# Kernel optimization log

Hardware: AMD Instinct MI355X
Metric: run time of the kernel (lower is better)

The kernel has to match this reference:

```python
import jax, jax.numpy as jnp
import numpy as np
from jax import lax

ALPHA = 0.95
THRESH = 1.0
DN = ('NCDHW', 'OIDHW', 'NCDHW')  # (batch, chan, T, H, W)


def lif(x):
    # x: [B, C, T, H, W]. y[t] = (1-a)*y_reset[t-1] + x[t]; s = (y>=th); y *= (1-s)
    xt = jnp.moveaxis(x, 2, 0)  # [T, B, C, H, W]

    def step(y, x_t):
        y = (1.0 - ALPHA) * y + x_t
        s = (y >= THRESH).astype(x.dtype)
        return y * (1.0 - s), s

    _, s = lax.scan(step, jnp.zeros_like(xt[0]), xt)
    return jnp.moveaxis(s, 0, 2)  # back to [B, C, T, H, W]


def delta_encode(x):
    # temporal difference along T (axis 2), zero-padded at t=0
    d = x[:, :, 1:] - x[:, :, :-1]
    return jnp.concatenate([jnp.zeros_like(x[:, :, :1]), d], axis=2)


def setup_inputs() -> dict:
    key = jax.random.key(0)
    ks = jax.random.split(key, 7)
    B, H, W, T = 2, 64, 64, 350
    return {
        'x': jax.random.uniform(ks[0], (B, 2, H, W, T), dtype=jnp.float32),
        'conv1_w': jax.random.normal(ks[1], (8, 2, 5, 5, 1), dtype=jnp.float32) * 0.1,
        'conv1_b': jax.random.normal(ks[2], (8,), dtype=jnp.float32) * 0.1,
        'deconv_w': jax.random.normal(ks[3], (2, 8, 2, 2, 1), dtype=jnp.float32) * 0.1,
        'deconv_b': jax.random.normal(ks[4], (2,), dtype=jnp.float32) * 0.1,
        'conv2_w': jax.random.normal(ks[5], (2, 2), dtype=jnp.float32) * 0.1,
        'conv2_b': jax.random.normal(ks[6], (2,), dtype=jnp.float32) * 0.1,
    }


def reference(x, conv1_w, conv1_b, deconv_w, deconv_b, conv2_w, conv2_b):
    # x: [B, 2, H, W, T] -> [B, 2, T, H, W]
    h = jnp.transpose(x, (0, 1, 4, 2, 3))
    # conv1: kernel (5,5,1) over (T,H,W), padding (2,2,0)
    h = lax.conv_general_dilated(h, conv1_w, (1, 1, 1),
                                 [(2, 2), (2, 2), (0, 0)],
                                 dimension_numbers=DN)
    h = jax.nn.relu(h + conv1_b[None, :, None, None, None])
    h = lif(h)
    h = delta_encode(h)
    # deconv: kernel (2,2,1), stride (2,2,1) -> upsamples T and H by 2
    h = lax.conv_transpose(h, deconv_w, (2, 2, 1), 'VALID',
                           dimension_numbers=DN)
    h = h + deconv_b[None, :, None, None, None]
    # dropout3d(0.1) is identity in eval mode
    h = jax.nn.relu(h)
    # conv2: 1x1x1 conv == channel-mixing matmul
    h = jnp.einsum('oc,bcthw->bothw', conv2_w, h) + conv2_b[None, :, None, None, None]
    h = lif(h)
    # [B, C, T', H', W'] -> [B, C, H', W', T']
    return jnp.transpose(h, (0, 1, 3, 4, 2))
```

## Files before the change

### kernel.cpp

```cpp
#include <hip/hip_runtime.h>

constexpr int B  = 2,  CIN = 2,  H = 64, W = 64, T = 350;
constexpr int C1 = 8;
constexpr int TO = 700, HO = 128, WO = 64;
constexpr int HW = H * W;

#define DEC 0.05000000074505806f

__global__ void __launch_bounds__(256) transpose_kernel(
    const float* __restrict__ x, float* __restrict__ xT) {
  __shared__ float tile[64][65];
  int bid   = blockIdx.x;
  int tTile = bid % 6;
  int slice = bid / 6;
  int h  = slice % H;
  int bc = slice / H;
  int t0 = tTile * 64;
  int tx = threadIdx.x & 63;
  int tz = threadIdx.x >> 6;

  const float* src = x + ((long)bc * H + h) * (long)(W * T);
#pragma unroll
  for (int i = 0; i < 16; ++i) {
    int w = tz * 16 + i;
    int t = t0 + tx;
    tile[w][tx] = (t < T) ? src[(long)w * T + t] : 0.0f;
  }
  __syncthreads();
  float* dst = xT + ((long)bc * T) * HW + h * 64;
#pragma unroll
  for (int i = 0; i < 16; ++i) {
    int tl = tz * 16 + i;
    int t  = t0 + tl;
    if (t < T) dst[(long)t * HW + tx] = tile[tx][tl];
  }
}

__device__ __forceinline__ void gload_lds16(const float* g, float* l) {
  __builtin_amdgcn_global_load_lds(
      (const __attribute__((address_space(1))) unsigned int*)g,
      (__attribute__((address_space(3))) unsigned int*)l, 16, 0, 0);
}

__global__ void __launch_bounds__(512) convlif_kernel(
    const float* __restrict__ xT, const float* __restrict__ w1,
    const float* __restrict__ b1, signed char* __restrict__ d8) {
  __shared__ float buf[2][128 * 64];
  const int tid = threadIdx.x;
  const int bid = blockIdx.x;
  const int chunk = bid & 3;
  const int rest  = bid >> 2;
  const int h = rest & 63;
  const int b = rest >> 6;
  const int w  = tid & 63;
  const int co = tid >> 6;

  float wt[2][5][5];
#pragma unroll
  for (int ci = 0; ci < 2; ++ci)
#pragma unroll
    for (int dt = 0; dt < 5; ++dt)
#pragma unroll
      for (int dh = 0; dh < 5; ++dh)
        wt[ci][dt][dh] = w1[((co * 2 + ci) * 5 + dt) * 5 + dh];
  float bias = b1[co];

  const float* basep[2][5];
#pragma unroll
  for (int ci = 0; ci < 2; ++ci)
#pragma unroll
    for (int dh = 0; dh < 5; ++dh) {
      int hh = h + dh - 2;
      bool hv = (hh >= 0) && (hh < H);
      int hc = hh < 0 ? 0 : (hh > H - 1 ? H - 1 : hh);
      basep[ci][dh] = xT + ((long)((b * 2 + ci) * T)) * HW + hc * 64 + w;
      if (!hv) {
#pragma unroll
        for (int dt = 0; dt < 5; ++dt) wt[ci][dt][dh] = 0.0f;
      }
    }

  int tloc[4];
  int cpart[4];
#pragma unroll
  for (int i = 0; i < 4; ++i) {
    int r = (tid >> 4) + 32 * i;
    if (r > 99) r = 99;
    int tl  = r / 10;
    int rem = r - tl * 10;
    int ci  = rem / 5;
    int dh  = rem - ci * 5;
    int hh = h + dh - 2;
    int hc = hh < 0 ? 0 : (hh > H - 1 ? H - 1 : hh);
    tloc[i]  = tl;
    cpart[i] = ((b * 2 + ci) * T) * HW + hc * 64 + (tid & 15) * 4;
  }

  const int tstore = chunk * 88;
  const int ts     = chunk ? tstore - 15 : 0;
  const int te     = tstore + 88 < T ? tstore + 88 : T;
  const int nsup   = (te - ts + 9) / 10;

  {
    int bs = ts + 3;
#pragma unroll
    for (int i = 0; i < 4; ++i) {
      int tau = bs + tloc[i];
      if (tau > T - 1) tau = T - 1;
      gload_lds16(xT + (long)cpart[i] + (long)tau * HW,
                  &buf[0][(i * 32 + co * 4) * 64]);
    }
  }

  float win[2][5][5];
#pragma unroll
  for (int ci = 0; ci < 2; ++ci)
#pragma unroll
    for (int dh = 0; dh < 5; ++dh) {
      const float* bp = basep[ci][dh];
      win[ci][dh][3] = (ts >= 2) ? bp[(long)(ts - 2) * HW] : 0.0f;
      win[ci][dh][4] = (ts >= 1) ? bp[(long)(ts - 1) * HW] : 0.0f;
      win[ci][dh][0] = bp[(long)(ts + 0) * HW];
      win[ci][dh][1] = bp[(long)(ts + 1) * HW];
      win[ci][dh][2] = bp[(long)(ts + 2) * HW];
    }

  asm volatile("s_waitcnt vmcnt(0)" ::: "memory");
  __builtin_amdgcn_s_barrier();
  asm volatile("" ::: "memory");

  signed char* dsto = d8 + ((long)(b * T) * HW + h * 64 + w) * C1 + co;

  float y = 0.0f, sprev = 0.0f;
  for (int k = 0; k < nsup; ++k) {
    asm volatile("" ::: "memory");
    __builtin_amdgcn_s_barrier();
    asm volatile("" ::: "memory");
    if (k + 1 < nsup) {
      int bs = ts + 3 + 10 * (k + 1);
      float* nb = &buf[(k + 1) & 1][0];
#pragma unroll
      for (int i = 0; i < 4; ++i) {
        int tau = bs + tloc[i];
        if (tau > T - 1) tau = T - 1;
        gload_lds16(xT + (long)cpart[i] + (long)tau * HW,
                    nb + (i * 32 + co * 4) * 64);
      }
      asm volatile("s_waitcnt vmcnt(4)" ::: "memory");
    } else {
      asm volatile("s_waitcnt vmcnt(0)" ::: "memory");
    }
    __builtin_amdgcn_s_barrier();
    asm volatile("" ::: "memory");

    float* lb = &buf[k & 1][0];
    {
      int bufstart = ts + 3 + 10 * k;
      int rz0 = (T - bufstart) * 10;
      if (rz0 < 100) {
        if (rz0 < 0) rz0 = 0;
        for (int r = rz0 + co; r < 100; r += 8) lb[r * 64 + w] = 0.0f;
        asm volatile("" ::: "memory");
        __builtin_amdgcn_s_barrier();
        asm volatile("" ::: "memory");
      }
    }

    const int t0s = ts + 10 * k;
    for (int jj = 0; jj < 2; ++jj) {
#pragma unroll
      for (int u = 0; u < 5; ++u) {
        const int j5 = jj * 5;
        int t = t0s + j5 + u;
        float ac0 = 0.f, ac1 = 0.f, ac2 = 0.f, ac3 = 0.f;
#pragma unroll
        for (int ci = 0; ci < 2; ++ci)
#pragma unroll
          for (int dt = 0; dt < 5; ++dt) {
            const int slot = (u + dt + 3) % 5;
#pragma unroll
            for (int dh = 0; dh < 5; ++dh) {
              const int q = (ci * 25 + dt * 5 + dh) & 3;
              float p = win[ci][dh][slot] * wt[ci][dt][dh];
              if (q == 0) ac0 += p;
              else if (q == 1) ac1 += p;
              else if (q == 2) ac2 += p;
              else ac3 += p;
            }
          }
        float a = ((ac0 + ac1) + (ac2 + ac3)) + bias;
        a = fmaxf(a, 0.0f);
        y = fmaf(DEC, y, a);
        float s = (y >= 1.0f) ? 1.0f : 0.0f;
        if (t >= tstore && t < te) {
          float dlt = (t == 0) ? 0.0f : (s - sprev);
          dsto[(long)t * (HW * C1)] = (signed char)dlt;
        }
        sprev = s;
        y = (s != 0.0f) ? 0.0f : y;
        const int slot2 = (u + 3) % 5;
#pragma unroll
        for (int ci = 0; ci < 2; ++ci)
#pragma unroll
          for (int dh = 0; dh < 5; ++dh)
            win[ci][dh][slot2] = lb[((j5 + u) * 10 + ci * 5 + dh) * 64 + w];
      }
    }
  }
}

__global__ void __launch_bounds__(64) stage2_kernel(
    const signed char* __restrict__ d8, const float* __restrict__ dw,
    const float* __restrict__ db, const float* __restrict__ cw,
    const float* __restrict__ cb, float* __restrict__ out) {
  __shared__ float SB[2][64][17];
  int bid   = blockIdx.x;
  int chunk = bid & 15;
  int rest  = bid >> 4;
  int hp = rest & 127;
  int b  = rest >> 7;
  int wp = threadIdx.x;

  int h  = hp >> 1;
  int kh = 1 - (hp & 1);

  float dwk0[2][8], dwk1[2][8];
#pragma unroll
  for (int c = 0; c < 2; ++c)
#pragma unroll
    for (int ci = 0; ci < 8; ++ci) {
      dwk0[c][ci] = dw[((c * 8 + ci) * 2 + 0) * 2 + kh];
      dwk1[c][ci] = dw[((c * 8 + ci) * 2 + 1) * 2 + kh];
    }
  float db0 = db[0], db1 = db[1];
  float cw00 = cw[0], cw01 = cw[1], cw10 = cw[2], cw11 = cw[3];
  float cb0 = cb[0], cb1 = cb[1];

  int t0 = chunk * 44;
  int t1 = (t0 + 44 < TO) ? t0 + 44 : TO;
  int tw = (t0 - 16 > 0) ? t0 - 16 : 0;

  const signed char* dbase = d8 + (((long)b * T) * HW + h * 64 + wp) * C1;
  const long tstride = (long)HW * C1;
  float* outb = out + ((long)b * 2 * HO) * (long)(WO * TO);

  float y0 = 0.0f, y1 = 0.0f;
  uint2 dc = *reinterpret_cast<const uint2*>(dbase + (long)(tw >> 1) * tstride);
  for (int tp = tw; tp < t1; tp += 2) {
    int tn = (tp + 2 < t1) ? ((tp + 2) >> 1) : ((t1 - 1) >> 1);
    uint2 dn = *reinterpret_cast<const uint2*>(dbase + (long)tn * tstride);

    float dv[8];
#pragma unroll
    for (int ci = 0; ci < 4; ++ci) {
      dv[ci]     = (float)(signed char)((dc.x >> (8 * ci)) & 0xff);
      dv[ci + 4] = (float)(signed char)((dc.y >> (8 * ci)) & 0xff);
    }

#pragma unroll
    for (int par = 0; par < 2; ++par) {
      int tpp = tp + par;
      float v0 = db0, v1 = db1;
      if (par == 0) {
#pragma unroll
        for (int ci = 0; ci < 8; ++ci) {
          v0 = fmaf(dv[ci], dwk1[0][ci], v0);
          v1 = fmaf(dv[ci], dwk1[1][ci], v1);
        }
      } else {
#pragma unroll
        for (int ci = 0; ci < 8; ++ci) {
          v0 = fmaf(dv[ci], dwk0[0][ci], v0);
          v1 = fmaf(dv[ci], dwk0[1][ci], v1);
        }
      }
      v0 = fmaxf(v0, 0.0f);
      v1 = fmaxf(v1, 0.0f);
      float u0 = fmaf(cw00, v0, fmaf(cw01, v1, cb0));
      float u1 = fmaf(cw10, v0, fmaf(cw11, v1, cb1));
      y0 = fmaf(DEC, y0, u0);
      y1 = fmaf(DEC, y1, u1);
      float s0 = (y0 >= 1.0f) ? 1.0f : 0.0f;
      float s1 = (y1 >= 1.0f) ? 1.0f : 0.0f;
      y0 = (s0 != 0.0f) ? 0.0f : y0;
      y1 = (s1 != 0.0f) ? 0.0f : y1;

      if (tpp >= t0) {
        int k = (tpp - t0) & 15;
        SB[0][wp][k] = s0;
        SB[1][wp][k] = s1;
        if (par == 1 && (k == 15 || tpp == t1 - 1)) {
          __syncthreads();
          int Kc  = k + 1;
          int t0f = tpp - k;
#pragma unroll
          for (int o = 0; o < 2; ++o) {
            float* ob = outb + ((long)(o * HO + hp)) * (long)(WO * TO);
#pragma unroll
            for (int i = 0; i < 4; ++i) {
              int idx = (i << 6) + wp;
              int r   = idx >> 2;
              int c   = (idx & 3) << 2;
              if (c < Kc) {
                float4 vv;
                vv.x = SB[o][r][c + 0];
                vv.y = SB[o][r][c + 1];
                vv.z = SB[o][r][c + 2];
                vv.w = SB[o][r][c + 3];
                *reinterpret_cast<float4*>(ob + (long)r * TO + (t0f + c)) = vv;
              }
            }
          }
          __syncthreads();
        }
      }
    }
    dc = dn;
  }
}

extern "C" void kernel_launch(void* const* d_in, const int* in_sizes, int n_in,
                              void* d_out, int out_size, void* d_ws, size_t ws_size,
                              hipStream_t stream) {
  const float* x  = (const float*)d_in[0];
  const float* w1 = (const float*)d_in[1];
  const float* b1 = (const float*)d_in[2];
  const float* dw = (const float*)d_in[3];
  const float* db = (const float*)d_in[4];
  const float* cw = (const float*)d_in[5];
  const float* cb = (const float*)d_in[6];
  float* out = (float*)d_out;

  float* xT = (float*)d_ws;
  signed char* d8 = (signed char*)d_ws + (size_t)B * CIN * T * HW * 4;

  transpose_kernel<<<dim3(B * CIN * H * 6), dim3(256), 0, stream>>>(x, xT);
  convlif_kernel<<<dim3(B * H * 4), dim3(512), 0, stream>>>(xT, w1, b1, d8);
  stage2_kernel<<<dim3(B * HO * 16), dim3(64), 0, stream>>>(d8, dw, db, cw, cb, out);
}
```

Measured before the change: 121.6 us.

## Process two H rows and two output channels per thread in conv-LIF kernel

Each conv-LIF block now covers two adjacent H rows, and each thread computes two output channels, so every input tap loaded into registers feeds twice the FMAs. The LDS staging holds 6 H rows per channel instead of 5, letting both rows share one time window. Spike deltas are packed into an LDS staging tile and written to global memory as 16-byte vector stores, replacing scattered byte stores. The grid drops to 256 blocks, which lowers parallelism, and register pressure rises from the doubled weights and accumulators.

Result: faster. 104.0 us (-14.5%).

```diff
diff --git a/kernel.cpp b/kernel.cpp
--- a/kernel.cpp
+++ b/kernel.cpp
@@ -46,70 +46,60 @@
     const float* __restrict__ xT, const float* __restrict__ w1,
     const float* __restrict__ b1, signed char* __restrict__ d8) {
   __shared__ float buf[2][128 * 64];
+  __shared__ __align__(16) unsigned char st[10][1024];
   const int tid = threadIdx.x;
   const int bid = blockIdx.x;
   const int chunk = bid & 3;
   const int rest  = bid >> 2;
-  const int h = rest & 63;
-  const int b = rest >> 6;
+  const int h2 = rest & 31;
+  const int b  = rest >> 5;
+  const int h0 = h2 * 2;
   const int w  = tid & 63;
-  const int co = tid >> 6;
-
-  float wt[2][5][5];
-#pragma unroll
-  for (int ci = 0; ci < 2; ++ci)
-#pragma unroll
-    for (int dt = 0; dt < 5; ++dt)
-#pragma unroll
-      for (int dh = 0; dh < 5; ++dh)
-        wt[ci][dt][dh] = w1[((co * 2 + ci) * 5 + dt) * 5 + dh];
-  float bias = b1[co];
-
-  const float* basep[2][5];
+  const int hs = (tid >> 6) & 1;
+  const int cp = tid >> 7;
+  const int h  = h0 + hs;
+  const int wid = tid >> 6;
+
+  const int tstore = chunk * 90;
+  const int ts     = chunk ? tstore - 15 : 0;
+  const int te     = tstore + 90 < T ? tstore + 90 : T;
+  const int nsup   = (te - ts + 9) / 10;
+
+  float wt[2][2][5][5];
 #pragma unroll
   for (int ci = 0; ci < 2; ++ci)
 #pragma unroll
     for (int dh = 0; dh < 5; ++dh) {
       int hh = h + dh - 2;
       bool hv = (hh >= 0) && (hh < H);
-      int hc = hh < 0 ? 0 : (hh > H - 1 ? H - 1 : hh);
-      basep[ci][dh] = xT + ((long)((b * 2 + ci) * T)) * HW + hc * 64 + w;
-      if (!hv) {
-#pragma unroll
-        for (int dt = 0; dt < 5; ++dt) wt[ci][dt][dh] = 0.0f;
-      }
-    }
-
-  int tloc[4];
-  int cpart[4];
+#pragma unroll
+      for (int dt = 0; dt < 5; ++dt) {
+        wt[0][ci][dt][dh] = hv ? w1[(((cp*2+0) * 2 + ci) * 5 + dt) * 5 + dh] : 0.0f;
+        wt[1][ci][dt][dh] = hv ? w1[(((cp*2+1) * 2 + ci) * 5 + dt) * 5 + dh] : 0.0f;
+      }
+    }
+  float bias0 = b1[cp*2], bias1 = b1[cp*2+1];
+
+  int cdesc[4];
 #pragma unroll
   for (int i = 0; i < 4; ++i) {
     int r = (tid >> 4) + 32 * i;
-    if (r > 99) r = 99;
-    int tl  = r / 10;
-    int rem = r - tl * 10;
-    int ci  = rem / 5;
-    int dh  = rem - ci * 5;
-    int hh = h + dh - 2;
+    if (r > 119) r = 119;
+    int j   = r / 12;
+    int rem = r - j * 12;
+    int ci  = rem / 6;
+    int dhh = rem - ci * 6;
+    int hh = h0 + dhh - 2;
     int hc = hh < 0 ? 0 : (hh > H - 1 ? H - 1 : hh);
-    tloc[i]  = tl;
-    cpart[i] = ((b * 2 + ci) * T) * HW + hc * 64 + (tid & 15) * 4;
-  }
-
-  const int tstore = chunk * 88;
-  const int ts     = chunk ? tstore - 15 : 0;
-  const int te     = tstore + 88 < T ? tstore + 88 : T;
-  const int nsup   = (te - ts + 9) / 10;
-
-  {
-    int bs = ts + 3;
-#pragma unroll
-    for (int i = 0; i < 4; ++i) {
-      int tau = bs + tloc[i];
-      if (tau > T - 1) tau = T - 1;
-      gload_lds16(xT + (long)cpart[i] + (long)tau * HW,
-                  &buf[0][(i * 32 + co * 4) * 64]);
-    }
+    cdesc[i] = (((b * 2 + ci) * T) * HW + hc * 64 + (tid & 15) * 4) | (j << 27);
+  }
+
+#pragma unroll
+  for (int i = 0; i < 4; ++i) {
+    int tau = ts + 3 + (cdesc[i] >> 27);
+    if (tau > T - 1) tau = T - 1;
+    gload_lds16(xT + (long)(cdesc[i] & 0x07ffffff) + (long)tau * HW,
+                &buf[0][(i * 32 + wid * 4) * 64]);
   }
 
   float win[2][5][5];
@@ -117,7 +107,9 @@
   for (int ci = 0; ci < 2; ++ci)
 #pragma unroll
     for (int dh = 0; dh < 5; ++dh) {
-      const float* bp = basep[ci][dh];
+      int hh = h + dh - 2;
+      int hc = hh < 0 ? 0 : (hh > H - 1 ? H - 1 : hh);
+      const float* bp = xT + ((long)((b * 2 + ci) * T)) * HW + hc * 64 + w;
       win[ci][dh][3] = (ts >= 2) ? bp[(long)(ts - 2) * HW] : 0.0f;
       win[ci][dh][4] = (ts >= 1) ? bp[(long)(ts - 1) * HW] : 0.0f;
       win[ci][dh][0] = bp[(long)(ts + 0) * HW];
@@ -129,38 +121,58 @@
   __builtin_amdgcn_s_barrier();
   asm volatile("" ::: "memory");
 
-  signed char* dsto = d8 + ((long)(b * T) * HW + h * 64 + w) * C1 + co;
-
-  float y = 0.0f, sprev = 0.0f;
+  signed char* const d8row = d8 + ((long)(b * T)) * (HW * C1) + h0 * 512;
+  const int stw = ((hs * 64 + w) * 8 + cp * 2) >> 1;
+
+  float y0 = 0.0f, y1 = 0.0f, sp0 = 0.0f, sp1 = 0.0f;
   for (int k = 0; k < nsup; ++k) {
-    asm volatile("" ::: "memory");
+    asm volatile("s_waitcnt lgkmcnt(0)" ::: "memory");
     __builtin_amdgcn_s_barrier();
     asm volatile("" ::: "memory");
+
+    if (k > 0) {
+      int tb = ts + 10 * (k - 1);
+#pragma unroll
+      for (int i = 0; i < 2; ++i) {
+        int slot = tid + i * 512;
+        if (slot < 640) {
+          int u = slot >> 6;
+          int c = (slot & 63) * 16;
+          int t = tb + u;
+          if (t >= tstore && t < te) {
+            uint4 v = *reinterpret_cast<const uint4*>(&st[u][c]);
+            *reinterpret_cast<uint4*>(d8row + (long)t * (HW * C1) + c) = v;
+          }
+        }
+      }
+    }
+
     if (k + 1 < nsup) {
       int bs = ts + 3 + 10 * (k + 1);
       float* nb = &buf[(k + 1) & 1][0];
 #pragma unroll
       for (int i = 0; i < 4; ++i) {
-        int tau = bs + tloc[i];
+        int tau = bs + (cdesc[i] >> 27);
         if (tau > T - 1) tau = T - 1;
-        gload_lds16(xT + (long)cpart[i] + (long)tau * HW,
-                    nb + (i * 32 + co * 4) * 64);
+        gload_lds16(xT + (long)(cdesc[i] & 0x07ffffff) + (long)tau * HW,
+                    nb + (i * 32 + wid * 4) * 64);
       }
       asm volatile("s_waitcnt vmcnt(4)" ::: "memory");
     } else {
       asm volatile("s_waitcnt vmcnt(0)" ::: "memory");
     }
+    asm volatile("s_waitcnt lgkmcnt(0)" ::: "memory");
     __builtin_amdgcn_s_barrier();
     asm volatile("" ::: "memory");
 
     float* lb = &buf[k & 1][0];
     {
       int bufstart = ts + 3 + 10 * k;
-      int rz0 = (T - bufstart) * 10;
-      if (rz0 < 100) {
+      int rz0 = (T - bufstart) * 12;
+      if (rz0 < 120) {
         if (rz0 < 0) rz0 = 0;
-        for (int r = rz0 + co; r < 100; r += 8) lb[r * 64 + w] = 0.0f;
-        asm volatile("" ::: "memory");
+        for (int r = rz0 + wid; r < 120; r += 8) lb[r * 64 + w] = 0.0f;
+        asm volatile("s_waitcnt lgkmcnt(0)" ::: "memory");
         __builtin_amdgcn_s_barrier();
         asm volatile("" ::: "memory");
       }
@@ -172,7 +184,8 @@
       for (int u = 0; u < 5; ++u) {
         const int j5 = jj * 5;
         int t = t0s + j5 + u;
-        float ac0 = 0.f, ac1 = 0.f, ac2 = 0.f, ac3 = 0.f;
+        float a0q0 = 0.f, a0q1 = 0.f, a0q2 = 0.f, a0q3 = 0.f;
+        float a1q0 = 0.f, a1q1 = 0.f, a1q2 = 0.f, a1q3 = 0.f;
 #pragma unroll
         for (int ci = 0; ci < 2; ++ci)
 #pragma unroll
@@ -181,29 +194,56 @@
 #pragma unroll
             for (int dh = 0; dh < 5; ++dh) {
               const int q = (ci * 25 + dt * 5 + dh) & 3;
-              float p = win[ci][dh][slot] * wt[ci][dt][dh];
-              if (q == 0) ac0 += p;
-              else if (q == 1) ac1 += p;
-              else if (q == 2) ac2 += p;
-              else ac3 += p;
+              float tap = win[ci][dh][slot];
+              float p0 = tap * wt[0][ci][dt][dh];
+              float p1 = tap * wt[1][ci][dt][dh];
+              if (q == 0)      { a0q0 += p0; a1q0 += p1; }
+              else if (q == 1) { a0q1 += p0; a1q1 += p1; }
+              else if (q == 2) { a0q2 += p0; a1q2 += p1; }
+              else             { a0q3 += p0; a1q3 += p1; }
             }
           }
-        float a = ((ac0 + ac1) + (ac2 + ac3)) + bias;
-        a = fmaxf(a, 0.0f);
-        y = fmaf(DEC, y, a);
-        float s = (y >= 1.0f) ? 1.0f : 0.0f;
+        float a0 = fmaxf(((a0q0 + a0q1) + (a0q2 + a0q3)) + bias0, 0.0f);
+        float a1 = fmaxf(((a1q0 + a1q1) + (a1q2 + a1q3)) + bias1, 0.0f);
+        y0 = fmaf(DEC, y0, a0);
+        y1 = fmaf(DEC, y1, a1);
+        float s0 = (y0 >= 1.0f) ? 1.0f : 0.0f;
+        float s1 = (y1 >= 1.0f) ? 1.0f : 0.0f;
+        int d0 = (int)(s0 - sp0) & 0xff;
+        int d1 = (int)(s1 - sp1) & 0xff;
+        unsigned short val = (unsigned short)(d0 | (d1 << 8));
+        if (t == 0) val = 0;
+        reinterpret_cast<unsigned short*>(&st[j5 + u][0])[stw] = val;
+        sp0 = s0; sp1 = s1;
+        y0 = (s0 != 0.0f) ? 0.0f : y0;
+        y1 = (s1 != 0.0f) ? 0.0f : y1;
+        const int slot2 = (u + 3) % 5;
+#pragma unroll
+        for (int ci = 0; ci < 2; ++ci)
+#pragma unroll
+          for (int dh = 0; dh < 5; ++dh)
+            win[ci][dh][slot2] =
+                lb[((j5 + u) * 12 + ci * 6 + dh + hs) * 64 + w];
+      }
+    }
+  }
+
+  asm volatile("s_waitcnt lgkmcnt(0)" ::: "memory");
+  __builtin_amdgcn_s_barrier();
+  asm volatile("" ::: "memory");
+  {
+    int tb = ts + 10 * (nsup - 1);
+#pragma unroll
+    for (int i = 0; i < 2; ++i) {
+      int slot = tid + i * 512;
+      if (slot < 640) {
+        int u = slot >> 6;
+        int c = (slot & 63) * 16;
+        int t = tb + u;
         if (t >= tstore && t < te) {
-          float dlt = (t == 0) ? 0.0f : (s - sprev);
-          dsto[(long)t * (HW * C1)] = (signed char)dlt;
-        }
-        sprev = s;
-        y = (s != 0.0f) ? 0.0f : y;
-        const int slot2 = (u + 3) % 5;
-#pragma unroll
-        for (int ci = 0; ci < 2; ++ci)
-#pragma unroll
-          for (int dh = 0; dh < 5; ++dh)
-            win[ci][dh][slot2] = lb[((j5 + u) * 10 + ci * 5 + dh) * 64 + w];
+          uint4 v = *reinterpret_cast<const uint4*>(&st[u][c]);
+          *reinterpret_cast<uint4*>(d8row + (long)t * (HW * C1) + c) = v;
+        }
       }
     }
   }
@@ -335,6 +375,6 @@
   signed char* d8 = (signed char*)d_ws + (size_t)B * CIN * T * HW * 4;
 
   transpose_kernel<<<dim3(B * CIN * H * 6), dim3(256), 0, stream>>>(x, xT);
-  convlif_kernel<<<dim3(B * H * 4), dim3(512), 0, stream>>>(xT, w1, b1, d8);
+  convlif_kernel<<<dim3(B * 32 * 4), dim3(512), 0, stream>>>(xT, w1, b1, d8);
   stage2_kernel<<<dim3(B * HO * 16), dim3(64), 0, stream>>>(d8, dw, db, cw, cb, out);
 }
```
